# Performance work log

Hardware: AMD Instinct MI355X
Metric: run time of the kernel (lower is better)

The kernel has to match this reference:

```python
import jax, jax.numpy as jnp
import numpy as np

B = 8192
D_IN = 512
UNITS = 512


def setup_inputs() -> dict:
    key = jax.random.key(0)
    ks = jax.random.split(key, 9)
    sx = 1.0 / np.sqrt(D_IN)
    sh = 1.0 / np.sqrt(UNITS)
    return {
        "input_x": jax.random.normal(ks[0], (B, D_IN), jnp.float32),
        "input_h": jax.random.normal(ks[1], (B, UNITS), jnp.float32),
        "attention_score": jax.random.uniform(ks[2], (B, 1), jnp.float32),
        "Wx_r": jax.random.normal(ks[3], (D_IN, UNITS), jnp.float32) * sx,
        "b_r": jnp.zeros((UNITS,), jnp.float32),
        "Wh_r": jax.random.normal(ks[4], (UNITS, UNITS), jnp.float32) * sh,
        "Wx_u": jax.random.normal(ks[5], (D_IN, UNITS), jnp.float32) * sx,
        "b_u": jnp.zeros((UNITS,), jnp.float32),
        "Wh_u": jax.random.normal(ks[6], (UNITS, UNITS), jnp.float32) * sh,
        "Wx_h": jax.random.normal(ks[7], (D_IN, UNITS), jnp.float32) * sx,
        "b_h": jnp.zeros((UNITS,), jnp.float32),
        "Wh_h": jax.random.normal(ks[8], (UNITS, UNITS), jnp.float32) * sh,
    }


def reference(input_x, input_h, attention_score,
              Wx_r, b_r, Wh_r,
              Wx_u, b_u, Wh_u,
              Wx_h, b_h, Wh_h):
    # reset gate: sigmoid(Dense_b(x) + Dense(h))
    r = jax.nn.sigmoid(input_x @ Wx_r + b_r + input_h @ Wh_r)
    # update gate: sigmoid(Dense_b(x) + Dense(h))
    u = jax.nn.sigmoid(input_x @ Wx_u + b_u + input_h @ Wh_u)
    # candidate: tanh(Dense_b(x) + r * Dense(h))
    cal_h = jnp.tanh(input_x @ Wx_h + b_h + r * (input_h @ Wh_h))
    # attention-modulated update and interpolation
    u_att = attention_score * u
    h = (1.0 - u_att) * input_h + u_att * cal_h
    return h
```

## Files before the change

kernel.cpp:

```cpp
#include <hip/hip_runtime.h>
#include <hip/hip_bf16.h>

typedef __bf16 bf16x8 __attribute__((ext_vector_type(8)));
typedef float f32x4 __attribute__((ext_vector_type(4)));
typedef unsigned short us8 __attribute__((ext_vector_type(8)));

#define MFMA16 __builtin_amdgcn_mfma_f32_16x16x32_bf16

__device__ __forceinline__ unsigned short f2bf(float f) {
    unsigned int u = __float_as_uint(f);
    u += 0x7fffu + ((u >> 16) & 1u);
    return (unsigned short)(u >> 16);
}

__device__ __forceinline__ void gload_lds16(const void* g, void* l) {
    __builtin_amdgcn_global_load_lds(
        (const __attribute__((address_space(1))) unsigned int*)g,
        (__attribute__((address_space(3))) unsigned int*)l, 16, 0, 0);
}

__global__ void cvt_all_kernel(const float* __restrict__ x, const float* __restrict__ h,
                               unsigned short* __restrict__ AP,
                               const float* __restrict__ W0, const float* __restrict__ W1,
                               const float* __restrict__ W2, const float* __restrict__ W3,
                               const float* __restrict__ W4, const float* __restrict__ W5,
                               unsigned short* __restrict__ WP) {
    if (blockIdx.x < 4096) {
        int c = blockIdx.x * 256 + threadIdx.x;
        int ih = c >> 19;
        const float* src = ih ? h : x;
        int c2 = c & 524287;
        int mb = c2 >> 10, kb = (c2 >> 6) & 15, lane = c2 & 63;
        int r = lane & 15, ko = lane >> 4;
        const float* p = src + (size_t)(mb * 16 + r) * 512 + kb * 32 + ko * 8;
        float4 v0 = *(const float4*)p;
        float4 v1 = *(const float4*)(p + 4);
        us8 o = { f2bf(v0.x), f2bf(v0.y), f2bf(v0.z), f2bf(v0.w),
                  f2bf(v1.x), f2bf(v1.y), f2bf(v1.z), f2bf(v1.w) };
        *((us8*)AP + ((size_t)(mb * 32 + kb + ih * 16) << 6) + lane) = o;
    } else {
        int c = (blockIdx.x - 4096) * 256 + threadIdx.x;
        int s = c >> 16, c2 = c & 65535;
        int frag = c2 >> 6, lane = c2 & 63;
        int nb = frag >> 5, kbp = frag & 31;
        const float* Wsrc;
        int kb;
        if (kbp < 16) { kb = kbp;      Wsrc = (s == 0) ? W0 : (s == 1) ? W2 : W4; }
        else          { kb = kbp - 16; Wsrc = (s == 0) ? W1 : (s == 1) ? W3 : W5; }
        int cc = lane & 15, ko = lane >> 4;
        int kbase = kb * 32 + ko * 8;
        us8 o;
#pragma unroll
        for (int e = 0; e < 8; ++e)
            o[e] = f2bf(Wsrc[(size_t)(kbase + e) * 512 + nb * 16 + cc]);
        *((us8*)WP + c) = o;
    }
}

__global__ __launch_bounds__(512, 2) void augru_mm(
    const unsigned short* __restrict__ AP_,
    const unsigned short* __restrict__ WP_,
    const float* __restrict__ b_r, const float* __restrict__ b_u, const float* __restrict__ b_h,
    const float* __restrict__ att, const float* __restrict__ h32,
    float* __restrict__ out) {
    __shared__ unsigned char sL[2][57344];
    const unsigned char* AP  = (const unsigned char*)AP_;
    const unsigned char* WPb = (const unsigned char*)WP_;

    const int t = threadIdx.x, wv = t >> 6, lane = t & 63;
    const int laneoff = lane * 16;

    const int bid = blockIdx.x;
    const int Wid = (bid & 7) * 32 + (bid >> 3);
    const int mblk = Wid >> 3, nblk = Wid & 7;
    const int wr = wv >> 1, wc = wv & 1;

    f32x4 accR[4][2] = {}, accU[4][2] = {}, accXH[4][2] = {}, accHH[4][2] = {};

    const unsigned char* gsrc[7];
    unsigned ldst[7];
#pragma unroll
    for (int i = 0; i < 4; ++i) {
        int f = i * 8 + wv, mbL = f >> 1, kq = f & 1;
        gsrc[i] = AP + ((size_t)((mblk * 16 + mbL) * 32 + kq) << 10) + laneoff;
        ldst[i] = (unsigned)f << 10;
    }
#pragma unroll
    for (int i = 4; i < 7; ++i) {
        int g = (i - 4) * 8 + wv, s = g >> 3, nbL = (g >> 1) & 3, kq = g & 1;
        gsrc[i] = WPb + (size_t)s * 1048576 +
                  ((size_t)((nblk * 4 + nbL) * 32 + kq) << 10) + laneoff;
        ldst[i] = 32768u + ((unsigned)g << 10);
    }

    unsigned aoff[4], boff[3][2];
#pragma unroll
    for (int mf = 0; mf < 4; ++mf) aoff[mf] = (((wr * 4 + mf) * 2) << 10) + laneoff;
#pragma unroll
    for (int s = 0; s < 3; ++s)
#pragma unroll
        for (int nf = 0; nf < 2; ++nf)
            boff[s][nf] = 32768u + (((s * 4 + wc * 2 + nf) * 2) << 10) + laneoff;

#define ISSUE(kk, bufi) { _Pragma("unroll") for (int i = 0; i < 7; ++i) \
        gload_lds16(gsrc[i] + ((size_t)(kk) << 11), &sL[bufi][ldst[i]]); }

#define WAITBAR(n) asm volatile("s_waitcnt vmcnt(" #n ")\n\ts_barrier" ::: "memory");
#define RELBAR     asm volatile("s_waitcnt lgkmcnt(0)\n\ts_barrier" ::: "memory");

#define COMPUTE(bufp, ACCC) { _Pragma("unroll") for (int kq = 0; kq < 2; ++kq) { \
        bf16x8 ax[4]; \
        _Pragma("unroll") for (int mf = 0; mf < 4; ++mf) \
            ax[mf] = *(const bf16x8*)((bufp) + aoff[mf] + (kq << 10)); \
        bf16x8 bR[2], bU[2], bC[2]; \
        _Pragma("unroll") for (int nf = 0; nf < 2; ++nf) { \
            bR[nf] = *(const bf16x8*)((bufp) + boff[0][nf] + (kq << 10)); \
            bU[nf] = *(const bf16x8*)((bufp) + boff[1][nf] + (kq << 10)); \
            bC[nf] = *(const bf16x8*)((bufp) + boff[2][nf] + (kq << 10)); } \
        __builtin_amdgcn_s_setprio(1); \
        _Pragma("unroll") for (int mf = 0; mf < 4; ++mf) \
            _Pragma("unroll") for (int nf = 0; nf < 2; ++nf) { \
                accR[mf][nf] = MFMA16(ax[mf], bR[nf], accR[mf][nf], 0, 0, 0); \
                accU[mf][nf] = MFMA16(ax[mf], bU[nf], accU[mf][nf], 0, 0, 0); \
                ACCC[mf][nf] = MFMA16(ax[mf], bC[nf], ACCC[mf][nf], 0, 0, 0); } \
        __builtin_amdgcn_s_setprio(0); } }

    ISSUE(0, 0)
    ISSUE(1, 1)

#pragma unroll 1
    for (int k = 0; k < 8; ++k) {
        unsigned char* bufp = &sL[k & 1][0];
        WAITBAR(7)
        COMPUTE(bufp, accXH)
        RELBAR
        ISSUE(k + 2, k & 1)
    }
#pragma unroll 1
    for (int k = 8; k < 14; ++k) {
        unsigned char* bufp = &sL[k & 1][0];
        WAITBAR(7)
        COMPUTE(bufp, accHH)
        RELBAR
        ISSUE(k + 2, k & 1)
    }
    {   unsigned char* bufp = &sL[0][0];
        WAITBAR(7)
        COMPUTE(bufp, accHH)
        RELBAR }
    {   unsigned char* bufp = &sL[1][0];
        WAITBAR(0)
        COMPUTE(bufp, accHH) }

    const int lr = lane & 15, lg = lane >> 4;
#pragma unroll
    for (int nf = 0; nf < 2; ++nf) {
        const int col = nblk * 64 + wc * 32 + nf * 16 + lr;
        const float br = b_r[col], bu = b_u[col], bh = b_h[col];
#pragma unroll
        for (int mf = 0; mf < 4; ++mf) {
            const int rowb = mblk * 256 + wr * 64 + mf * 16 + lg * 4;
#pragma unroll
            for (int q = 0; q < 4; ++q) {
                const int row = rowb + q;
                float r = 1.f / (1.f + __expf(-(accR[mf][nf][q] + br)));
                float u = 1.f / (1.f + __expf(-(accU[mf][nf][q] + bu)));
                float ph = accXH[mf][nf][q] + bh + r * accHH[mf][nf][q];
                ph = fminf(fmaxf(ph, -15.f), 15.f);
                float e = __expf(2.f * ph);
                float cal = (e - 1.f) / (e + 1.f);
                float hv = h32[(size_t)row * 512 + col];
                float ua = att[row] * u;
                out[(size_t)row * 512 + col] = fmaf(ua, cal - hv, hv);
            }
        }
    }
#undef ISSUE
#undef WAITBAR
#undef RELBAR
#undef COMPUTE
}

extern "C" void kernel_launch(void* const* d_in, const int* in_sizes, int n_in,
                              void* d_out, int out_size, void* d_ws, size_t ws_size,
                              hipStream_t stream) {
    const float* x    = (const float*)d_in[0];
    const float* h    = (const float*)d_in[1];
    const float* att  = (const float*)d_in[2];
    const float* Wx_r = (const float*)d_in[3];
    const float* b_r  = (const float*)d_in[4];
    const float* Wh_r = (const float*)d_in[5];
    const float* Wx_u = (const float*)d_in[6];
    const float* b_u  = (const float*)d_in[7];
    const float* Wh_u = (const float*)d_in[8];
    const float* Wx_h = (const float*)d_in[9];
    const float* b_h  = (const float*)d_in[10];
    const float* Wh_h = (const float*)d_in[11];
    float* out = (float*)d_out;

    unsigned short* AP = (unsigned short*)d_ws;
    unsigned short* WP = AP + 8388608;

    cvt_all_kernel<<<4864, 256, 0, stream>>>(x, h, AP,
        Wx_r, Wh_r, Wx_u, Wh_u, Wx_h, Wh_h, WP);
    augru_mm<<<256, 512, 0, stream>>>(AP, WP, b_r, b_u, b_h, att, h, out);
}
```

Baseline: 45.94 us.

## Split per-tile compute into barrier-synchronized ping-pong phases of LDS loads and MFMAs

Restructures each K-tile into four phases, each loading a few A/B fragments from LDS, then crossing a workgroup barrier, waiting on lgkmcnt and running 12 MFMAs at raised priority. The goal is to interleave LDS reads and MFMA bursts across the two waves per SIMD, HipKittens-style, and to keep register pressure lower by loading two A fragments at a time. The cost is many extra s_barriers per tile. Correctness relies on the barrier placement relative to the async global-to-LDS loads.

New measurement: 45.73 us. About the same (-0.5%).

```diff
diff --git a/kernel.cpp b/kernel.cpp
--- a/kernel.cpp
+++ b/kernel.cpp
@@ -102,55 +102,78 @@
         for (int nf = 0; nf < 2; ++nf)
             boff[s][nf] = 32768u + (((s * 4 + wc * 2 + nf) * 2) << 10) + laneoff;
 
-#define ISSUE(kk, bufi) { _Pragma("unroll") for (int i = 0; i < 7; ++i) \
-        gload_lds16(gsrc[i] + ((size_t)(kk) << 11), &sL[bufi][ldst[i]]); }
-
-#define WAITBAR(n) asm volatile("s_waitcnt vmcnt(" #n ")\n\ts_barrier" ::: "memory");
-#define RELBAR     asm volatile("s_waitcnt lgkmcnt(0)\n\ts_barrier" ::: "memory");
-
-#define COMPUTE(bufp, ACCC) { _Pragma("unroll") for (int kq = 0; kq < 2; ++kq) { \
-        bf16x8 ax[4]; \
-        _Pragma("unroll") for (int mf = 0; mf < 4; ++mf) \
-            ax[mf] = *(const bf16x8*)((bufp) + aoff[mf] + (kq << 10)); \
-        bf16x8 bR[2], bU[2], bC[2]; \
-        _Pragma("unroll") for (int nf = 0; nf < 2; ++nf) { \
-            bR[nf] = *(const bf16x8*)((bufp) + boff[0][nf] + (kq << 10)); \
-            bU[nf] = *(const bf16x8*)((bufp) + boff[1][nf] + (kq << 10)); \
-            bC[nf] = *(const bf16x8*)((bufp) + boff[2][nf] + (kq << 10)); } \
-        __builtin_amdgcn_s_setprio(1); \
-        _Pragma("unroll") for (int mf = 0; mf < 4; ++mf) \
-            _Pragma("unroll") for (int nf = 0; nf < 2; ++nf) { \
-                accR[mf][nf] = MFMA16(ax[mf], bR[nf], accR[mf][nf], 0, 0, 0); \
-                accU[mf][nf] = MFMA16(ax[mf], bU[nf], accU[mf][nf], 0, 0, 0); \
-                ACCC[mf][nf] = MFMA16(ax[mf], bC[nf], ACCC[mf][nf], 0, 0, 0); } \
-        __builtin_amdgcn_s_setprio(0); } }
+#define ISSUE(TT, BI) { _Pragma("unroll") for (int i = 0; i < 7; ++i) \
+        gload_lds16(gsrc[i] + ((size_t)(TT) << 11), &sL[BI][ldst[i]]); }
+
+#define VM7BAR asm volatile("s_waitcnt vmcnt(7)" ::: "memory"); \
+               __builtin_amdgcn_s_barrier();
+#define VM0BAR asm volatile("s_waitcnt vmcnt(0)" ::: "memory"); \
+               __builtin_amdgcn_s_barrier();
+
+#define LDA(mf, kq) (*(const bf16x8*)(bufp + aoff[mf] + ((kq) << 10)))
+#define LDB(s, nf, kq) (*(const bf16x8*)(bufp + boff[s][nf] + ((kq) << 10)))
+
+#define MM6(av, mf, nf, ACCC) \
+    accR[mf][nf] = MFMA16(av, bRr[nf], accR[mf][nf], 0, 0, 0); \
+    accU[mf][nf] = MFMA16(av, bUr[nf], accU[mf][nf], 0, 0, 0); \
+    ACCC[mf][nf] = MFMA16(av, bCr[nf], ACCC[mf][nf], 0, 0, 0);
+
+#define PH_MID \
+    __builtin_amdgcn_s_barrier(); \
+    asm volatile("s_waitcnt lgkmcnt(0)" ::: "memory"); \
+    __builtin_amdgcn_sched_barrier(0); \
+    __builtin_amdgcn_s_setprio(1);
+
+#define PH_END \
+    __builtin_amdgcn_s_setprio(0); \
+    __builtin_amdgcn_s_barrier();
+
+#define DO_TILE(BUFP, ACCC) { \
+    const unsigned char* bufp = (BUFP); \
+    bf16x8 a0, a1, bRr[2], bUr[2], bCr[2]; \
+     \
+    a0 = LDA(0, 0); a1 = LDA(1, 0); \
+    bRr[0] = LDB(0, 0, 0); bRr[1] = LDB(0, 1, 0); \
+    bUr[0] = LDB(1, 0, 0); bUr[1] = LDB(1, 1, 0); \
+    bCr[0] = LDB(2, 0, 0); bCr[1] = LDB(2, 1, 0); \
+    PH_MID MM6(a0, 0, 0, ACCC) MM6(a0, 0, 1, ACCC) \
+           MM6(a1, 1, 0, ACCC) MM6(a1, 1, 1, ACCC) PH_END \
+     \
+    a0 = LDA(2, 0); a1 = LDA(3, 0); \
+    PH_MID MM6(a0, 2, 0, ACCC) MM6(a0, 2, 1, ACCC) \
+           MM6(a1, 3, 0, ACCC) MM6(a1, 3, 1, ACCC) PH_END \
+     \
+    a0 = LDA(0, 1); a1 = LDA(1, 1); \
+    bRr[0] = LDB(0, 0, 1); bRr[1] = LDB(0, 1, 1); \
+    bUr[0] = LDB(1, 0, 1); bUr[1] = LDB(1, 1, 1); \
+    bCr[0] = LDB(2, 0, 1); bCr[1] = LDB(2, 1, 1); \
+    PH_MID MM6(a0, 0, 0, ACCC) MM6(a0, 0, 1, ACCC) \
+           MM6(a1, 1, 0, ACCC) MM6(a1, 1, 1, ACCC) PH_END \
+     \
+    a0 = LDA(2, 1); a1 = LDA(3, 1); \
+    PH_MID MM6(a0, 2, 0, ACCC) MM6(a0, 2, 1, ACCC) \
+           MM6(a1, 3, 0, ACCC) MM6(a1, 3, 1, ACCC) PH_END \
+}
 
     ISSUE(0, 0)
     ISSUE(1, 1)
+    VM7BAR
 
 #pragma unroll 1
-    for (int k = 0; k < 8; ++k) {
-        unsigned char* bufp = &sL[k & 1][0];
-        WAITBAR(7)
-        COMPUTE(bufp, accXH)
-        RELBAR
-        ISSUE(k + 2, k & 1)
+    for (int tt = 0; tt < 8; ++tt) {
+        DO_TILE(&sL[tt & 1][0], accXH)
+        ISSUE(tt + 2, tt & 1)
+        VM7BAR
     }
 #pragma unroll 1
-    for (int k = 8; k < 14; ++k) {
-        unsigned char* bufp = &sL[k & 1][0];
-        WAITBAR(7)
-        COMPUTE(bufp, accHH)
-        RELBAR
-        ISSUE(k + 2, k & 1)
-    }
-    {   unsigned char* bufp = &sL[0][0];
-        WAITBAR(7)
-        COMPUTE(bufp, accHH)
-        RELBAR }
-    {   unsigned char* bufp = &sL[1][0];
-        WAITBAR(0)
-        COMPUTE(bufp, accHH) }
+    for (int tt = 8; tt < 14; ++tt) {
+        DO_TILE(&sL[tt & 1][0], accHH)
+        ISSUE(tt + 2, tt & 1)
+        VM7BAR
+    }
+    DO_TILE(&sL[0][0], accHH)
+    VM0BAR
+    DO_TILE(&sL[1][0], accHH)
 
     const int lr = lane & 15, lg = lane >> 4;
 #pragma unroll
@@ -176,9 +199,14 @@
         }
     }
 #undef ISSUE
-#undef WAITBAR
-#undef RELBAR
-#undef COMPUTE
+#undef VM7BAR
+#undef VM0BAR
+#undef LDA
+#undef LDB
+#undef MM6
+#undef PH_MID
+#undef PH_END
+#undef DO_TILE
 }
 
 extern "C" void kernel_launch(void* const* d_in, const int* in_sizes, int n_in,
```

## Replace barrier-synced shared LDS pipeline with per-wave private A staging and register-loaded B

Applied to the files above, without the earlier changes.

Each wave now stages only its own A fragments into a private LDS region through global_load_lds, double buffered at 32-wide K granularity. B fragments are loaded straight from global memory into registers, double buffered. This removes the block-wide s_barrier and the cross-wave sharing of staged tiles, so waves progress independently. The trade is more global/L2 traffic, since B fragments are no longer shared through LDS and waves in the same row or column each fetch their own copy. Register pressure also rises from holding two sets of B registers.

New measurement: 48.72 us. 6.0% more time.

```diff
diff --git a/kernel.cpp b/kernel.cpp
--- a/kernel.cpp
+++ b/kernel.cpp
@@ -63,11 +63,11 @@
     const float* __restrict__ b_r, const float* __restrict__ b_u, const float* __restrict__ b_h,
     const float* __restrict__ att, const float* __restrict__ h32,
     float* __restrict__ out) {
-    __shared__ unsigned char sL[2][57344];
-    const unsigned char* AP  = (const unsigned char*)AP_;
+    __shared__ unsigned char sA[65536];
+    const unsigned char* APb = (const unsigned char*)AP_;
     const unsigned char* WPb = (const unsigned char*)WP_;
 
-    const int t = threadIdx.x, wv = t >> 6, lane = t & 63;
+    const int t0 = threadIdx.x, wv = t0 >> 6, lane = t0 & 63;
     const int laneoff = lane * 16;
 
     const int bid = blockIdx.x;
@@ -77,80 +77,78 @@
 
     f32x4 accR[4][2] = {}, accU[4][2] = {}, accXH[4][2] = {}, accHH[4][2] = {};
 
-    const unsigned char* gsrc[7];
-    unsigned ldst[7];
-#pragma unroll
-    for (int i = 0; i < 4; ++i) {
-        int f = i * 8 + wv, mbL = f >> 1, kq = f & 1;
-        gsrc[i] = AP + ((size_t)((mblk * 16 + mbL) * 32 + kq) << 10) + laneoff;
-        ldst[i] = (unsigned)f << 10;
-    }
-#pragma unroll
-    for (int i = 4; i < 7; ++i) {
-        int g = (i - 4) * 8 + wv, s = g >> 3, nbL = (g >> 1) & 3, kq = g & 1;
-        gsrc[i] = WPb + (size_t)s * 1048576 +
-                  ((size_t)((nblk * 4 + nbL) * 32 + kq) << 10) + laneoff;
-        ldst[i] = 32768u + ((unsigned)g << 10);
-    }
-
-    unsigned aoff[4], boff[3][2];
-#pragma unroll
-    for (int mf = 0; mf < 4; ++mf) aoff[mf] = (((wr * 4 + mf) * 2) << 10) + laneoff;
+    const unsigned char* gA[4];
+    unsigned dsA[4];
+#pragma unroll
+    for (int mf = 0; mf < 4; ++mf) {
+        int mb = mblk * 16 + wr * 4 + mf;
+        gA[mf] = APb + ((size_t)(mb * 32) << 10) + laneoff;
+        dsA[mf] = (unsigned)(wv * 8192 + mf * 1024);
+    }
+    const unsigned char* gB[3][2];
 #pragma unroll
     for (int s = 0; s < 3; ++s)
 #pragma unroll
         for (int nf = 0; nf < 2; ++nf)
-            boff[s][nf] = 32768u + (((s * 4 + wc * 2 + nf) * 2) << 10) + laneoff;
-
-#define ISSUE(kk, bufi) { _Pragma("unroll") for (int i = 0; i < 7; ++i) \
-        gload_lds16(gsrc[i] + ((size_t)(kk) << 11), &sL[bufi][ldst[i]]); }
-
-#define WAITBAR(n) asm volatile("s_waitcnt vmcnt(" #n ")\n\ts_barrier" ::: "memory");
-#define RELBAR     asm volatile("s_waitcnt lgkmcnt(0)\n\ts_barrier" ::: "memory");
-
-#define COMPUTE(bufp, ACCC) { _Pragma("unroll") for (int kq = 0; kq < 2; ++kq) { \
-        bf16x8 ax[4]; \
-        _Pragma("unroll") for (int mf = 0; mf < 4; ++mf) \
-            ax[mf] = *(const bf16x8*)((bufp) + aoff[mf] + (kq << 10)); \
-        bf16x8 bR[2], bU[2], bC[2]; \
-        _Pragma("unroll") for (int nf = 0; nf < 2; ++nf) { \
-            bR[nf] = *(const bf16x8*)((bufp) + boff[0][nf] + (kq << 10)); \
-            bU[nf] = *(const bf16x8*)((bufp) + boff[1][nf] + (kq << 10)); \
-            bC[nf] = *(const bf16x8*)((bufp) + boff[2][nf] + (kq << 10)); } \
-        __builtin_amdgcn_s_setprio(1); \
-        _Pragma("unroll") for (int mf = 0; mf < 4; ++mf) \
-            _Pragma("unroll") for (int nf = 0; nf < 2; ++nf) { \
-                accR[mf][nf] = MFMA16(ax[mf], bR[nf], accR[mf][nf], 0, 0, 0); \
-                accU[mf][nf] = MFMA16(ax[mf], bU[nf], accU[mf][nf], 0, 0, 0); \
-                ACCC[mf][nf] = MFMA16(ax[mf], bC[nf], ACCC[mf][nf], 0, 0, 0); } \
-        __builtin_amdgcn_s_setprio(0); } }
-
-    ISSUE(0, 0)
-    ISSUE(1, 1)
+            gB[s][nf] = WPb + (size_t)s * 1048576 +
+                        ((size_t)((nblk * 4 + wc * 2 + nf) * 32) << 10) + laneoff;
+
+    bf16x8 a[4], b0[3][2], b1[3][2];
+
+#pragma unroll
+    for (int mf = 0; mf < 4; ++mf)
+        gload_lds16(gA[mf], (unsigned char*)sA + dsA[mf]);
+    asm volatile("" ::: "memory");
+#pragma unroll
+    for (int s = 0; s < 3; ++s)
+#pragma unroll
+        for (int nf = 0; nf < 2; ++nf)
+            b0[s][nf] = *(const bf16x8*)(gB[s][nf]);
+    asm volatile("" ::: "memory");
+#pragma unroll
+    for (int mf = 0; mf < 4; ++mf)
+        gload_lds16(gA[mf] + 1024, (unsigned char*)sA + dsA[mf] + 4096);
+    asm volatile("" ::: "memory");
+#pragma unroll
+    for (int s = 0; s < 3; ++s)
+#pragma unroll
+        for (int nf = 0; nf < 2; ++nf)
+            b1[s][nf] = *(const bf16x8*)(gB[s][nf] + 1024);
+
+#define BODY(T, P, BREG, ACCC, VMC, PF) { \
+    asm volatile("s_waitcnt vmcnt(" VMC ")" ::: "memory"); \
+    _Pragma("unroll") for (int mf = 0; mf < 4; ++mf) \
+        a[mf] = *(const bf16x8*)((const unsigned char*)sA + dsA[mf] + (P) * 4096 + laneoff); \
+    asm volatile("s_waitcnt lgkmcnt(0)" ::: "memory"); \
+    if (PF) { _Pragma("unroll") for (int mf = 0; mf < 4; ++mf) \
+        gload_lds16(gA[mf] + ((size_t)((T) + 2) << 10), \
+                    (unsigned char*)sA + dsA[mf] + (P) * 4096); } \
+    __builtin_amdgcn_s_setprio(1); \
+    _Pragma("unroll") for (int mf = 0; mf < 4; ++mf) \
+      _Pragma("unroll") for (int nf = 0; nf < 2; ++nf) { \
+        accR[mf][nf] = MFMA16(a[mf], BREG[0][nf], accR[mf][nf], 0, 0, 0); \
+        accU[mf][nf] = MFMA16(a[mf], BREG[1][nf], accU[mf][nf], 0, 0, 0); \
+        ACCC[mf][nf] = MFMA16(a[mf], BREG[2][nf], ACCC[mf][nf], 0, 0, 0); } \
+    __builtin_amdgcn_s_setprio(0); \
+    if (PF) { _Pragma("unroll") for (int s = 0; s < 3; ++s) \
+      _Pragma("unroll") for (int nf = 0; nf < 2; ++nf) \
+        BREG[s][nf] = *(const bf16x8*)(gB[s][nf] + ((size_t)((T) + 2) << 10)); } \
+}
 
 #pragma unroll 1
-    for (int k = 0; k < 8; ++k) {
-        unsigned char* bufp = &sL[k & 1][0];
-        WAITBAR(7)
-        COMPUTE(bufp, accXH)
-        RELBAR
-        ISSUE(k + 2, k & 1)
+    for (int i = 0; i < 8; ++i) {
+        const int te = 2 * i;
+        BODY(te,     0, b0, accXH, "10", true)
+        BODY(te + 1, 1, b1, accXH, "10", true)
     }
 #pragma unroll 1
-    for (int k = 8; k < 14; ++k) {
-        unsigned char* bufp = &sL[k & 1][0];
-        WAITBAR(7)
-        COMPUTE(bufp, accHH)
-        RELBAR
-        ISSUE(k + 2, k & 1)
-    }
-    {   unsigned char* bufp = &sL[0][0];
-        WAITBAR(7)
-        COMPUTE(bufp, accHH)
-        RELBAR }
-    {   unsigned char* bufp = &sL[1][0];
-        WAITBAR(0)
-        COMPUTE(bufp, accHH) }
+    for (int i = 8; i < 15; ++i) {
+        const int te = 2 * i;
+        BODY(te,     0, b0, accHH, "10", true)
+        BODY(te + 1, 1, b1, accHH, "10", true)
+    }
+    BODY(30, 0, b0, accHH, "10", false)
+    BODY(31, 1, b1, accHH, "0",  false)
 
     const int lr = lane & 15, lg = lane >> 4;
 #pragma unroll
@@ -175,10 +173,7 @@
             }
         }
     }
-#undef ISSUE
-#undef WAITBAR
-#undef RELBAR
-#undef COMPUTE
+#undef BODY
 }
 
 extern "C" void kernel_launch(void* const* d_in, const int* in_sizes, int n_in,
```
